# Kernel tuning notes

Measured on AMD Instinct MI355X. Metric: run time of the kernel, lower is better.

The kernel has to match this reference:

```python
import jax, jax.numpy as jnp
import numpy as np

B, C, H, W = 8, 64, 256, 512
FOV = np.pi / 4.0
KH = KW = 3


def _sphere_indices(H, W, fov):
    """Nearest-neighbor gather indices for a 3x3 spherical (gnomonic) kernel
    of angular extent `fov` on an equirectangular grid. Returns int32 [H, W, 9]."""
    taps = [(p, q) for p in (-1, 0, 1) for q in (-1, 0, 1)]
    theta = (0.5 - (np.arange(H) + 0.5) / H) * np.pi            # latitude per row [H]
    phi = ((np.arange(W) + 0.5) / W - 0.5) * 2.0 * np.pi        # longitude per col [W]
    r = np.tan(fov / 2.0)                                       # tangent-plane half extent
    gi_l, gj_l = [], []
    for (p, q) in taps:
        y_t, x_t = p * r, q * r
        rho = np.hypot(x_t, y_t)
        if rho == 0.0:
            lat = theta
            lon_off = np.zeros_like(theta)
        else:
            nu = np.arctan(rho)
            lat = np.arcsin(np.clip(np.cos(nu) * np.sin(theta)
                                    + y_t * np.sin(nu) * np.cos(theta) / rho, -1.0, 1.0))
            lon_off = np.arctan2(x_t * np.sin(nu),
                                 rho * np.cos(theta) * np.cos(nu)
                                 - y_t * np.sin(theta) * np.sin(nu))
        lon = phi[None, :] + lon_off[:, None]                   # [H, W]
        gi = np.clip(np.round((0.5 - lat / np.pi) * H - 0.5), 0, H - 1).astype(np.int32)
        gi = np.broadcast_to(gi[:, None], (H, W)).copy()
        gj = (np.round((lon / (2.0 * np.pi) + 0.5) * W - 0.5).astype(np.int64) % W).astype(np.int32)
        gi_l.append(gi)
        gj_l.append(gj)
    return np.stack(gi_l, axis=-1), np.stack(gj_l, axis=-1)    # [H, W, 9] each


def setup_inputs() -> dict:
    key = jax.random.key(0)
    k1, k2 = jax.random.split(key)
    feature = jax.random.normal(k1, (B, C, H, W), dtype=jnp.float32)
    weight = jax.random.normal(k2, (1, C, KH, KW), dtype=jnp.float32) * 0.05
    gi, gj = _sphere_indices(H, W, FOV)
    return {"feature": feature, "weight": weight,
            "gi": jnp.asarray(gi), "gj": jnp.asarray(gj)}


def reference(feature, weight, gi, gj):
    # SphericalConv: gather-based 3x3 conv over spherical sampling grid, stride 1, no bias.
    O, Cc, kh, kw = weight.shape
    wflat = weight.reshape(O, Cc, kh * kw)                      # [O, C, 9]
    Bb = feature.shape[0]
    Hh, Ww = gi.shape[0], gi.shape[1]
    out = jnp.zeros((Bb, O, Hh, Ww), feature.dtype)
    for k in range(kh * kw):                                    # fixed 9-tap loop
        xk = feature[:, :, gi[:, :, k], gj[:, :, k]]            # gather -> [B, C, H, W]
        out = out + jnp.einsum('bchw,oc->bohw', xk, wflat[:, :, k])
    # nn.Upsample(scale_factor=2) default nearest
    return jnp.repeat(jnp.repeat(out, 2, axis=2), 2, axis=3)
```

## Files before the change

### kernel.cpp

```cpp
#include <hip/hip_runtime.h>

#define Bn   8
#define Cn   64
#define Hn   256
#define Wn   512
#define HWn  (Hn * Wn)
#define TAPS 9

typedef float vfloat2 __attribute__((ext_vector_type(2)));

__global__ __launch_bounds__(256) void pass1_chandot(
    const float* __restrict__ feat, const float* __restrict__ wt,
    float* __restrict__ D)
{
    const int p = blockIdx.x * 256 + threadIdx.x;

    float acc[TAPS][Bn];
#pragma unroll
    for (int k = 0; k < TAPS; ++k)
#pragma unroll
        for (int b = 0; b < Bn; ++b) acc[k][b] = 0.f;

    float buf[2][4][Bn];

#pragma unroll
    for (int ci = 0; ci < 4; ++ci)
#pragma unroll
        for (int b = 0; b < Bn; ++b)
            buf[0][ci][b] = __builtin_nontemporal_load(
                feat + (size_t)(b * Cn + ci) * HWn + p);

#pragma unroll
    for (int g = 0; g < 16; ++g) {
        const int cur = g & 1, nxt = cur ^ 1;
        if (g < 15) {
            const int c0 = (g + 1) * 4;
#pragma unroll
            for (int ci = 0; ci < 4; ++ci)
#pragma unroll
                for (int b = 0; b < Bn; ++b)
                    buf[nxt][ci][b] = __builtin_nontemporal_load(
                        feat + (size_t)(b * Cn + c0 + ci) * HWn + p);
        }
#pragma unroll
        for (int ci = 0; ci < 4; ++ci) {
            const int c = g * 4 + ci;
#pragma unroll
            for (int k = 0; k < TAPS; ++k) {
                const float wv = wt[c * TAPS + k];
#pragma unroll
                for (int b = 0; b < Bn; ++b)
                    acc[k][b] = fmaf(buf[cur][ci][b], wv, acc[k][b]);
            }
        }
    }

#pragma unroll
    for (int k = 0; k < TAPS; ++k) {
        float4* dst = (float4*)(D + ((size_t)k * HWn + p) * Bn);
        dst[0] = make_float4(acc[k][0], acc[k][1], acc[k][2], acc[k][3]);
        dst[1] = make_float4(acc[k][4], acc[k][5], acc[k][6], acc[k][7]);
    }
}

__global__ __launch_bounds__(256) void pass2_gather(
    const float* __restrict__ D, const int* __restrict__ gi,
    const int* __restrict__ gj, float* __restrict__ out)
{
    __shared__ int loff[256 * TAPS];
    const int tid   = threadIdx.x;
    const int p0    = blockIdx.x * 256;
    const int gbase = p0 * TAPS;

#pragma unroll
    for (int i = tid; i < 256 * TAPS; i += 256)
        loff[i] = gi[gbase + i] * Wn + gj[gbase + i];
    __syncthreads();

    const int p = p0 + tid;
    const int w = p & (Wn - 1);
    const int h = p >> 9;

    float a[Bn];
#pragma unroll
    for (int b = 0; b < Bn; ++b) a[b] = 0.f;

#pragma unroll
    for (int k = 0; k < TAPS; ++k) {
        const int off = loff[tid * TAPS + k];
        const float4* d = (const float4*)(D + ((size_t)k * HWn + off) * Bn);
        float4 d0 = d[0], d1 = d[1];
        a[0] += d0.x; a[1] += d0.y; a[2] += d0.z; a[3] += d0.w;
        a[4] += d1.x; a[5] += d1.y; a[6] += d1.z; a[7] += d1.w;
    }

#pragma unroll
    for (int b = 0; b < Bn; ++b) {
        vfloat2 vv = {a[b], a[b]};
        size_t o = ((size_t)b * (2 * Hn) + 2 * h) * (size_t)(2 * Wn) + 2 * w;
        __builtin_nontemporal_store(vv, (vfloat2*)(out + o));
        __builtin_nontemporal_store(vv, (vfloat2*)(out + o + 2 * Wn));
    }
}

__global__ __launch_bounds__(256) void direct_kernel(
    const float* __restrict__ feat, const float* __restrict__ wt,
    const int* __restrict__ gi, const int* __restrict__ gj,
    float* __restrict__ out)
{
    int p = blockIdx.x * blockDim.x + threadIdx.x;
    int w = p & (Wn - 1);
    int h = (p >> 9) & (Hn - 1);
    int b = p >> 17;

    int iidx = ((h << 9) | w) * TAPS;
    int off[TAPS];
#pragma unroll
    for (int k = 0; k < TAPS; ++k)
        off[k] = gi[iidx + k] * Wn + gj[iidx + k];

    float acc = 0.f;
    for (int c = 0; c < Cn; ++c) {
        const float* fc = feat + ((size_t)b * Cn + c) * HWn;
#pragma unroll
        for (int k = 0; k < TAPS; ++k)
            acc = fmaf(fc[off[k]], wt[c * TAPS + k], acc);
    }

    float2 v = make_float2(acc, acc);
    size_t o0 = ((size_t)b * (2 * Hn) + 2 * h) * (size_t)(2 * Wn) + 2 * w;
    *(float2*)(out + o0)          = v;
    *(float2*)(out + o0 + 2 * Wn) = v;
}

extern "C" void kernel_launch(void* const* d_in, const int* in_sizes, int n_in,
                              void* d_out, int out_size, void* d_ws, size_t ws_size,
                              hipStream_t stream) {
    const float* feat = (const float*)d_in[0];
    const float* wt   = (const float*)d_in[1];
    const int*   gi   = (const int*)d_in[2];
    const int*   gj   = (const int*)d_in[3];
    float*       out  = (float*)d_out;

    const size_t bytesD = (size_t)TAPS * HWn * Bn * sizeof(float);

    if (ws_size >= bytesD) {
        float* D = (float*)d_ws;
        pass1_chandot<<<HWn / 256, 256, 0, stream>>>(feat, wt, D);
        pass2_gather <<<HWn / 256, 256, 0, stream>>>(D, gi, gj, out);
    } else {
        direct_kernel<<<(Bn * HWn) / 256, 256, 0, stream>>>(feat, wt, gi, gj, out);
    }
}
```

Measured before the change: 364.9 us.

## Switch intermediate to tap-batch-planar layout with float4 pixel vectors per thread

Pass 1 now assigns each thread four adjacent pixels of one batch and loads them as float4 vectors, writing D in a [tap][batch][pixel] planar layout instead of [tap][pixel][batch]. Pass 2 is restructured so each block covers 32 pixels times 8 batches, with each thread gathering one scalar per tap and writing one batch's upsampled output. The intent is wider, fully coalesced feature loads and less register pressure in pass 1. In exchange, pass 2 gathers become scalar reads spread across batch planes, its output stores are less contiguous per wavefront, and it launches more blocks.

```diff
diff --git a/kernel.cpp b/kernel.cpp
--- a/kernel.cpp
+++ b/kernel.cpp
@@ -8,27 +8,27 @@
 #define TAPS 9
 
 typedef float vfloat2 __attribute__((ext_vector_type(2)));
+typedef float vfloat4 __attribute__((ext_vector_type(4)));
 
 __global__ __launch_bounds__(256) void pass1_chandot(
     const float* __restrict__ feat, const float* __restrict__ wt,
     float* __restrict__ D)
 {
-    const int p = blockIdx.x * 256 + threadIdx.x;
+    const int t = blockIdx.x * 256 + threadIdx.x;
+    const int b = t >> 15;
+    const int p = (t & 32767) << 2;
 
-    float acc[TAPS][Bn];
+    const float* fb = feat + (size_t)b * (Cn * (size_t)HWn) + p;
+
+    vfloat4 acc[TAPS];
 #pragma unroll
-    for (int k = 0; k < TAPS; ++k)
-#pragma unroll
-        for (int b = 0; b < Bn; ++b) acc[k][b] = 0.f;
+    for (int k = 0; k < TAPS; ++k) acc[k] = (vfloat4)0.f;
 
-    float buf[2][4][Bn];
-
+    vfloat4 buf[2][4];
 #pragma unroll
     for (int ci = 0; ci < 4; ++ci)
-#pragma unroll
-        for (int b = 0; b < Bn; ++b)
-            buf[0][ci][b] = __builtin_nontemporal_load(
-                feat + (size_t)(b * Cn + ci) * HWn + p);
+        buf[0][ci] = __builtin_nontemporal_load(
+            (const vfloat4*)(fb + (size_t)ci * HWn));
 
 #pragma unroll
     for (int g = 0; g < 16; ++g) {
@@ -37,70 +37,57 @@
             const int c0 = (g + 1) * 4;
 #pragma unroll
             for (int ci = 0; ci < 4; ++ci)
-#pragma unroll
-                for (int b = 0; b < Bn; ++b)
-                    buf[nxt][ci][b] = __builtin_nontemporal_load(
-                        feat + (size_t)(b * Cn + c0 + ci) * HWn + p);
+                buf[nxt][ci] = __builtin_nontemporal_load(
+                    (const vfloat4*)(fb + (size_t)(c0 + ci) * HWn));
         }
 #pragma unroll
         for (int ci = 0; ci < 4; ++ci) {
             const int c = g * 4 + ci;
+            const vfloat4 f = buf[cur][ci];
 #pragma unroll
             for (int k = 0; k < TAPS; ++k) {
                 const float wv = wt[c * TAPS + k];
-#pragma unroll
-                for (int b = 0; b < Bn; ++b)
-                    acc[k][b] = fmaf(buf[cur][ci][b], wv, acc[k][b]);
+                acc[k] += f * wv;
             }
         }
     }
 
 #pragma unroll
-    for (int k = 0; k < TAPS; ++k) {
-        float4* dst = (float4*)(D + ((size_t)k * HWn + p) * Bn);
-        dst[0] = make_float4(acc[k][0], acc[k][1], acc[k][2], acc[k][3]);
-        dst[1] = make_float4(acc[k][4], acc[k][5], acc[k][6], acc[k][7]);
-    }
+    for (int k = 0; k < TAPS; ++k)
+        *(vfloat4*)(D + (size_t)(k * Bn + b) * HWn + p) = acc[k];
 }
 
 __global__ __launch_bounds__(256) void pass2_gather(
     const float* __restrict__ D, const int* __restrict__ gi,
     const int* __restrict__ gj, float* __restrict__ out)
 {
-    __shared__ int loff[256 * TAPS];
-    const int tid   = threadIdx.x;
-    const int p0    = blockIdx.x * 256;
-    const int gbase = p0 * TAPS;
+    __shared__ int loff[32 * TAPS];
+    const int tid = threadIdx.x;
+    const int p0  = blockIdx.x * 32;
 
-#pragma unroll
-    for (int i = tid; i < 256 * TAPS; i += 256)
-        loff[i] = gi[gbase + i] * Wn + gj[gbase + i];
+    for (int i = tid; i < 32 * TAPS; i += 256) {
+        const int g = p0 * TAPS + i;
+        loff[i] = gi[g] * Wn + gj[g];
+    }
     __syncthreads();
 
-    const int p = p0 + tid;
-    const int w = p & (Wn - 1);
-    const int h = p >> 9;
+    const int px = tid & 31;
+    const int b  = tid >> 5;
+    const int p  = p0 + px;
+    const int w  = p & (Wn - 1);
+    const int h  = p >> 9;
 
-    float a[Bn];
-#pragma unroll
-    for (int b = 0; b < Bn; ++b) a[b] = 0.f;
-
+    float a = 0.f;
 #pragma unroll
     for (int k = 0; k < TAPS; ++k) {
-        const int off = loff[tid * TAPS + k];
-        const float4* d = (const float4*)(D + ((size_t)k * HWn + off) * Bn);
-        float4 d0 = d[0], d1 = d[1];
-        a[0] += d0.x; a[1] += d0.y; a[2] += d0.z; a[3] += d0.w;
-        a[4] += d1.x; a[5] += d1.y; a[6] += d1.z; a[7] += d1.w;
+        const int off = loff[px * TAPS + k];
+        a += D[(size_t)(k * Bn + b) * HWn + off];
     }
 
-#pragma unroll
-    for (int b = 0; b < Bn; ++b) {
-        vfloat2 vv = {a[b], a[b]};
-        size_t o = ((size_t)b * (2 * Hn) + 2 * h) * (size_t)(2 * Wn) + 2 * w;
-        __builtin_nontemporal_store(vv, (vfloat2*)(out + o));
-        __builtin_nontemporal_store(vv, (vfloat2*)(out + o + 2 * Wn));
-    }
+    vfloat2 vv = {a, a};
+    const size_t o = ((size_t)b * (2 * Hn) + 2 * h) * (size_t)(2 * Wn) + 2 * w;
+    __builtin_nontemporal_store(vv, (vfloat2*)(out + o));
+    __builtin_nontemporal_store(vv, (vfloat2*)(out + o + 2 * Wn));
 }
 
 __global__ __launch_bounds__(256) void direct_kernel(
@@ -142,12 +129,12 @@
     const int*   gj   = (const int*)d_in[3];
     float*       out  = (float*)d_out;
 
-    const size_t bytesD = (size_t)TAPS * HWn * Bn * sizeof(float);
+    const size_t bytesD = (size_t)TAPS * Bn * HWn * sizeof(float);
 
     if (ws_size >= bytesD) {
         float* D = (float*)d_ws;
-        pass1_chandot<<<HWn / 256, 256, 0, stream>>>(feat, wt, D);
-        pass2_gather <<<HWn / 256, 256, 0, stream>>>(D, gi, gj, out);
+        pass1_chandot<<<(Bn * HWn / 4) / 256, 256, 0, stream>>>(feat, wt, D);
+        pass2_gather <<<HWn / 32,            256, 0, stream>>>(D, gi, gj, out);
     } else {
         direct_kernel<<<(Bn * HWn) / 256, 256, 0, stream>>>(feat, wt, gi, gj, out);
     }
```

Measured after the change: 365.3 us. No clear change (+0.1%).
